# Kernel optimization log

Hardware: AMD Instinct MI355X
Metric: run time of the kernel (lower is better)

Reference implementation:

```python
import jax, jax.numpy as jnp
import numpy as np

# Module hyperparameters (from init_kwargs)
THRESHOLD_BASE = 1.0
TAU_MEM, TAU_SYN, TAU_ADAPT = 0.02, 0.005, 0.1
ADAPT_STRENGTH, HOMEO_RATE, DT = 0.1, 0.01, 0.001


def setup_inputs() -> dict:
    key = jax.random.key(0)
    B, F, T = 32, 8192, 128
    input_current = jax.random.normal(key, (B, F, T), dtype=jnp.float32)
    threshold_scale = jnp.ones((1,), dtype=jnp.float32)   # nn.Parameter(torch.ones(1))
    adaptation_bias = jnp.zeros((1,), dtype=jnp.float32)  # nn.Parameter(torch.zeros(1))
    return {"input_current": input_current,
            "threshold_scale": threshold_scale,
            "adaptation_bias": adaptation_bias}


def reference(input_current, threshold_scale, adaptation_bias):
    """Adaptive-threshold LIF neuron recurrence (AdaptiveThresholdLIFNeuron.forward).

    input_current: [B, F, T]
    Returns (spikes [B,F,T], membrane_trace [T], threshold_trace [T],
             final_firing_rate (scalar EMA), adaptation_state (scalar mean)).
    """
    B, F, T = input_current.shape
    dt = jnp.float32(DT)
    alpha = jnp.exp(-dt / TAU_MEM)   # membrane decay
    beta = jnp.exp(-dt / TAU_SYN)    # synaptic decay
    gamma = jnp.exp(-dt / TAU_ADAPT) # adaptation decay

    I_t = jnp.moveaxis(input_current, -1, 0)  # [T, B, F] for scan over time

    def step(carry, inp):
        membrane, synaptic, adaptation, ema = carry
        synaptic = beta * synaptic + inp
        membrane = alpha * membrane + synaptic
        # homeostatic component uses the running firing-rate EMA (scalar buffer)
        homeo = ADAPT_STRENGTH * jnp.maximum(ema - HOMEO_RATE, 0.0)
        adaptation = gamma * adaptation + (1.0 - gamma) * jax.lax.stop_gradient(membrane)
        threshold = (THRESHOLD_BASE * threshold_scale + homeo
                     + adaptation_bias + 0.1 * adaptation)  # [B, F]
        spike = (membrane >= threshold).astype(membrane.dtype)
        ema = 0.99 * ema + 0.01 * spike.mean()
        membrane = membrane - threshold * spike  # soft reset
        return (membrane, synaptic, adaptation, ema), (spike, membrane.mean(), threshold.mean())

    z = jnp.zeros((B, F), dtype=input_current.dtype)
    init = (z, z, z, jnp.zeros((), dtype=input_current.dtype))
    (membrane, synaptic, adaptation, ema), (spikes_t, mem_trace, thr_trace) = jax.lax.scan(step, init, I_t)

    spikes = jnp.moveaxis(spikes_t, 0, -1)  # [B, F, T]
    return spikes, mem_trace, thr_trace, ema, adaptation.mean()
```

## Files before the change

### kernel.cpp

```cpp
#include <hip/hip_runtime.h>
#include <math.h>

#pragma clang fp contract(off)

typedef unsigned int u32;

#define N_NEUR 262144
#define TT     128
#define OB     ((size_t)N_NEUR * TT)
#define PB     128
#define PT     512
#define NW     8
#define GUARD_MAX (1 << 16)

__device__ __forceinline__ float f4c(const float4 v, int c) {
  switch (c & 3) { case 0: return v.x; case 1: return v.y; case 2: return v.z; default: return v.w; }
}
__device__ __forceinline__ float wredf(float v) {
#pragma unroll
  for (int o = 32; o; o >>= 1) v += __shfl_xor(v, o);
  return v;
}
__device__ __forceinline__ int wredi(int v) {
#pragma unroll
  for (int o = 32; o; o >>= 1) v += __shfl_xor(v, o);
  return v;
}

__launch_bounds__(PT)
__global__ void snn_persist(const float* __restrict__ in, const float* __restrict__ tsp,
                            const float* __restrict__ abp, float* __restrict__ out,
                            u32* __restrict__ bits2, u32* __restrict__ g_cnt,
                            u32* __restrict__ g_tot, float* __restrict__ wm,
                            float* __restrict__ wt, float* __restrict__ wa)
{
#pragma clang fp contract(off)
  const int tid  = threadIdx.x;
  const int bid  = blockIdx.x;
  const int gtid = bid * PT + tid;
  const int lane = tid & 63;
  const int wv   = tid >> 6;

  const float alp = __uint_as_float(0x3F7383C5u);
  const float bet = __uint_as_float(0x3F519856u);
  const float gma = __uint_as_float(0x3F7D73E8u);
  const float omg = 1.0f - gma;
  const float tsv = tsp[0];
  const float abv = abp[0];

  float s0=0.f,s1=0.f,s2=0.f,s3=0.f;
  float m0=0.f,m1=0.f,m2=0.f,m3=0.f;
  float a0=0.f,a1=0.f,a2=0.f,a3=0.f;
  float ema = 0.f;
  float sc  = (tsv + 0.1f * fmaxf(ema - 0.01f, 0.0f)) + abv;

  __shared__ int   shc[NW];
  __shared__ float shm[NW];
  __shared__ u32   s_tot;

  const int n0 = gtid * 4;
  const float* r0 = in + (size_t)(n0 + 0) * TT;
  const float* r1 = in + (size_t)(n0 + 1) * TT;
  const float* r2 = in + (size_t)(n0 + 2) * TT;
  const float* r3 = in + (size_t)(n0 + 3) * TT;

#define STEPSYNC(I0, I1, I2, I3, T_) {                                         \
    s0 = __builtin_fmaf(bet, s0, (I0));                                        \
    m0 = __builtin_fmaf(alp, m0, s0);                                          \
    const float aw0 = omg * m0;                                                \
    a0 = __builtin_fmaf(gma, a0, aw0);                                         \
    const float th0 = __builtin_fmaf(0.1f, a0, sc);                            \
    const bool sp0 = (m0 >= th0); if (sp0) m0 = m0 - th0;                      \
    s1 = __builtin_fmaf(bet, s1, (I1));                                        \
    m1 = __builtin_fmaf(alp, m1, s1);                                          \
    const float aw1 = omg * m1;                                                \
    a1 = __builtin_fmaf(gma, a1, aw1);                                         \
    const float th1 = __builtin_fmaf(0.1f, a1, sc);                            \
    const bool sp1 = (m1 >= th1); if (sp1) m1 = m1 - th1;                      \
    s2 = __builtin_fmaf(bet, s2, (I2));                                        \
    m2 = __builtin_fmaf(alp, m2, s2);                                          \
    const float aw2 = omg * m2;                                                \
    a2 = __builtin_fmaf(gma, a2, aw2);                                         \
    const float th2 = __builtin_fmaf(0.1f, a2, sc);                            \
    const bool sp2 = (m2 >= th2); if (sp2) m2 = m2 - th2;                      \
    s3 = __builtin_fmaf(bet, s3, (I3));                                        \
    m3 = __builtin_fmaf(alp, m3, s3);                                          \
    const float aw3 = omg * m3;                                                \
    a3 = __builtin_fmaf(gma, a3, aw3);                                         \
    const float th3 = __builtin_fmaf(0.1f, a3, sc);                            \
    const bool sp3 = (m3 >= th3); if (sp3) m3 = m3 - th3;                      \
    int cnt = (int)sp0 + (int)sp1 + (int)sp2 + (int)sp3;                       \
    cnt = wredi(cnt);                                                          \
    if (lane == 0) shc[wv] = cnt;                                              \
    __syncthreads();                                                           \
    if (wv == 0 && lane == 0) {                                                \
      int bc = ((((((shc[0] + shc[1]) + shc[2]) + shc[3]) + shc[4])            \
                 + shc[5]) + shc[6]) + shc[7];                                 \
      __hip_atomic_store(&g_cnt[(size_t)(T_) * PB + bid], (u32)bc + 1u,        \
                         __ATOMIC_RELAXED, __HIP_MEMORY_SCOPE_AGENT);          \
    }                                                                          \
           \
    u32 nib = (u32)sp0 | ((u32)sp1 << 1) | ((u32)sp2 << 2) | ((u32)sp3 << 3);  \
    u32 word = nib << (4 * (tid & 7));                                         \
    word |= (u32)__shfl_xor((int)word, 1);                                     \
    word |= (u32)__shfl_xor((int)word, 2);                                     \
    word |= (u32)__shfl_xor((int)word, 4);                                     \
    if ((tid & 7) == 0) bits2[(size_t)(gtid >> 3) * TT + (T_)] = word;         \
    float msum = ((m0 + m1) + m2) + m3;                                        \
    float tsum = ((th0 + th1) + th2) + th3;                                    \
    msum = wredf(msum); tsum = wredf(tsum);                                    \
    if (lane == 0) {                                                           \
      wm[((size_t)(T_) * PB + bid) * NW + wv] = msum;                          \
      wt[((size_t)(T_) * PB + bid) * NW + wv] = tsum;                          \
    }                                                                          \
    if (wv == 0) {                                                             \
      if (bid == 0) {         \
        const u32* slots_ = g_cnt + (size_t)(T_) * PB;                         \
        u32 v0_, v1_; int gd_ = 0;                                             \
        while (1) {                                                            \
          v0_ = __hip_atomic_load(&slots_[lane],      __ATOMIC_RELAXED, __HIP_MEMORY_SCOPE_AGENT); \
          v1_ = __hip_atomic_load(&slots_[lane + 64], __ATOMIC_RELAXED, __HIP_MEMORY_SCOPE_AGENT); \
          if (__all(v0_ != 0u && v1_ != 0u)) break;                            \
          if (++gd_ > GUARD_MAX) break;                                        \
        }                                                                      \
        int ss_ = (int)(v0_ ? v0_ - 1u : 0u) + (int)(v1_ ? v1_ - 1u : 0u);     \
        ss_ = wredi(ss_);                                                      \
        if (lane == 0) {                                                       \
          __hip_atomic_store(&g_tot[(T_)], (u32)ss_ + 1u,                      \
                             __ATOMIC_RELAXED, __HIP_MEMORY_SCOPE_AGENT);      \
          s_tot = (u32)ss_;                                                    \
        }                                                                      \
      } else {           \
        u32 v_; int gd_ = 0;                                                   \
        while (1) {                                                            \
          v_ = __hip_atomic_load(&g_tot[(T_)], __ATOMIC_RELAXED, __HIP_MEMORY_SCOPE_AGENT); \
          if (v_ != 0u) break;                                                 \
          if (++gd_ > GUARD_MAX) break;                                        \
          __builtin_amdgcn_s_sleep(1);                                         \
        }                                                                      \
        if (lane == 0) s_tot = (v_ ? v_ - 1u : 0u);                            \
      }                                                                        \
    }                                                                          \
    __syncthreads();                                                           \
    const float mean_ = (float)s_tot * 3.814697265625e-06f;                    \
    ema = __builtin_fmaf(0.99f, ema, 0.01f * mean_);                           \
    sc  = (tsv + 0.1f * fmaxf(ema - 0.01f, 0.0f)) + abv;                       \
  }

#define LOADC(X0,X1,X2,X3,X4,X5,X6,X7, c) {            \
    X0 = *(const float4*)(r0 + (c) * 8);               \
    X1 = *(const float4*)(r0 + (c) * 8 + 4);           \
    X2 = *(const float4*)(r1 + (c) * 8);               \
    X3 = *(const float4*)(r1 + (c) * 8 + 4);           \
    X4 = *(const float4*)(r2 + (c) * 8);               \
    X5 = *(const float4*)(r2 + (c) * 8 + 4);           \
    X6 = *(const float4*)(r3 + (c) * 8);               \
    X7 = *(const float4*)(r3 + (c) * 8 + 4); }

#define DOCHUNK(X0,X1,X2,X3,X4,X5,X6,X7, c) {                     \
    _Pragma("unroll")                                             \
    for (int k = 0; k < 8; ++k) {                                 \
      const float i0_ = (k < 4) ? f4c(X0, k) : f4c(X1, k);        \
      const float i1_ = (k < 4) ? f4c(X2, k) : f4c(X3, k);        \
      const float i2_ = (k < 4) ? f4c(X4, k) : f4c(X5, k);        \
      const float i3_ = (k < 4) ? f4c(X6, k) : f4c(X7, k);        \
      STEPSYNC(i0_, i1_, i2_, i3_, (c) * 8 + k);                  \
    } }

  float4 A0,A1,A2,A3,A4,A5,A6,A7;
  float4 B0,B1,B2,B3,B4,B5,B6,B7;

  LOADC(A0,A1,A2,A3,A4,A5,A6,A7, 0);
  for (int cc = 0; cc < 8; ++cc) {
    LOADC(B0,B1,B2,B3,B4,B5,B6,B7, 2 * cc + 1);
    DOCHUNK(A0,A1,A2,A3,A4,A5,A6,A7, 2 * cc);
    if (cc < 7) LOADC(A0,A1,A2,A3,A4,A5,A6,A7, 2 * cc + 2);
    DOCHUNK(B0,B1,B2,B3,B4,B5,B6,B7, 2 * cc + 1);
  }
#undef DOCHUNK
#undef LOADC
#undef STEPSYNC

  float asum = ((a0 + a1) + a2) + a3;
  asum = wredf(asum);
  __syncthreads();
  if (lane == 0) shm[wv] = asum;
  __syncthreads();
  if (tid == 0) {
    float bs = 0.f;
    for (int w = 0; w < NW; ++w) bs += shm[w];
    wa[bid] = bs;
    if (bid == 0) out[OB + 256] = ema;
  }
}

__launch_bounds__(256)
__global__ void snn_finish(const float* __restrict__ wm, const float* __restrict__ wt,
                           const float* __restrict__ wa, float* __restrict__ out)
{
#pragma clang fp contract(off)
  const int tid = threadIdx.x;
  const float inv = 3.814697265625e-06f;
  if (tid < 128) {
    float s = 0.f;
    for (int j = 0; j < PB * NW; ++j) s += wm[(size_t)tid * PB * NW + j];
    out[OB + tid] = s * inv;
  } else {
    const int t = tid - 128;
    float s = 0.f;
    for (int j = 0; j < PB * NW; ++j) s += wt[(size_t)t * PB * NW + j];
    out[OB + 128 + t] = s * inv;
  }
  if (tid == 0) {
    float s = 0.f;
    for (int b = 0; b < PB; ++b) s += wa[b];
    out[OB + 257] = s * inv;
  }
}

__global__ void snn_expand(const u32* __restrict__ bits2, float* __restrict__ outF)
{
  const int gtid = blockIdx.x * blockDim.x + threadIdx.x;
  const int wave = gtid >> 6, lane = gtid & 63;
  const int nwaves = (gridDim.x * blockDim.x) >> 6;
  const int nloc = lane >> 5;
  const int tq   = lane & 31;
  for (int pair = wave; pair < N_NEUR / 2; pair += nwaves) {
    const int n = 2 * pair + nloc;
    const uint4 w = *(const uint4*)(bits2 + (size_t)(n >> 5) * TT + 4 * tq);
    const int b = n & 31;
    float4 f;
    f.x = (float)((w.x >> b) & 1u);
    f.y = (float)((w.y >> b) & 1u);
    f.z = (float)((w.z >> b) & 1u);
    f.w = (float)((w.w >> b) & 1u);
    ((float4*)outF)[(size_t)n * (TT / 4) + tq] = f;
  }
}

extern "C" void kernel_launch(void* const* d_in, const int* in_sizes, int n_in,
                              void* d_out, int out_size, void* d_ws, size_t ws_size,
                              hipStream_t stream)
{
  const float* in  = (const float*)d_in[0];
  const float* tsp = (const float*)d_in[1];
  const float* abp = (const float*)d_in[2];
  float* out = (float*)d_out;
  unsigned char* ws = (unsigned char*)d_ws;

  if (ws_size < 5310000u) return;

  u32*   bits2 = (u32*)(ws);
  float* wm    = (float*)(ws + 4194304);
  float* wt    = (float*)(ws + 4718592);
  u32*   g_cnt = (u32*)(ws + 5242880);
  u32*   g_tot = (u32*)(ws + 5308416);
  float* wa    = (float*)(ws + 5308928);

  hipMemsetAsync(g_cnt, 0, 66048, stream);

  snn_persist<<<dim3(PB), dim3(PT), 0, stream>>>(in, tsp, abp, out,
                                                 bits2, g_cnt, g_tot, wm, wt, wa);
  snn_finish<<<dim3(1), dim3(256), 0, stream>>>(wm, wt, wa, out);
  snn_expand<<<dim3(2048), dim3(256), 0, stream>>>(bits2, out);
}
```

Measured before the change: 392.1 us.

## Replace two-stage gather/broadcast grid barrier with single packed atomic counter

Each block now does one atomic add per timestep on a single per-step word. The add packs an arrival count in the low 8 bits and the block's spike count in the upper bits. All blocks then poll that one word until the arrival count reaches the block count. This removes the old scheme in which block 0 gathered per-block slots and republished the total, cutting one serialized cross-block hop from each of the 128 timesteps. In exchange, all blocks contend on one address for both the atomics and the polling.

```diff
diff --git a/kernel.cpp b/kernel.cpp
--- a/kernel.cpp
+++ b/kernel.cpp
@@ -30,9 +30,9 @@
 __launch_bounds__(PT)
 __global__ void snn_persist(const float* __restrict__ in, const float* __restrict__ tsp,
                             const float* __restrict__ abp, float* __restrict__ out,
-                            u32* __restrict__ bits2, u32* __restrict__ g_cnt,
-                            u32* __restrict__ g_tot, float* __restrict__ wm,
-                            float* __restrict__ wt, float* __restrict__ wa)
+                            u32* __restrict__ bits2, u32* __restrict__ g_acc,
+                            float* __restrict__ wm, float* __restrict__ wt,
+                            float* __restrict__ wa)
 {
 #pragma clang fp contract(off)
   const int tid  = threadIdx.x;
@@ -96,8 +96,8 @@
     if (wv == 0 && lane == 0) {                                                \
       int bc = ((((((shc[0] + shc[1]) + shc[2]) + shc[3]) + shc[4])            \
                  + shc[5]) + shc[6]) + shc[7];                                 \
-      __hip_atomic_store(&g_cnt[(size_t)(T_) * PB + bid], (u32)bc + 1u,        \
-                         __ATOMIC_RELAXED, __HIP_MEMORY_SCOPE_AGENT);          \
+      __hip_atomic_fetch_add(&g_acc[(T_)], 1u | ((u32)bc << 8),                \
+                             __ATOMIC_RELAXED, __HIP_MEMORY_SCOPE_AGENT);      \
     }                                                                          \
            \
     u32 nib = (u32)sp0 | ((u32)sp1 << 1) | ((u32)sp2 << 2) | ((u32)sp3 << 3);  \
@@ -113,33 +113,16 @@
       wm[((size_t)(T_) * PB + bid) * NW + wv] = msum;                          \
       wt[((size_t)(T_) * PB + bid) * NW + wv] = tsum;                          \
     }                                                                          \
-    if (wv == 0) {                                                             \
-      if (bid == 0) {         \
-        const u32* slots_ = g_cnt + (size_t)(T_) * PB;                         \
-        u32 v0_, v1_; int gd_ = 0;                                             \
-        while (1) {                                                            \
-          v0_ = __hip_atomic_load(&slots_[lane],      __ATOMIC_RELAXED, __HIP_MEMORY_SCOPE_AGENT); \
-          v1_ = __hip_atomic_load(&slots_[lane + 64], __ATOMIC_RELAXED, __HIP_MEMORY_SCOPE_AGENT); \
-          if (__all(v0_ != 0u && v1_ != 0u)) break;                            \
-          if (++gd_ > GUARD_MAX) break;                                        \
-        }                                                                      \
-        int ss_ = (int)(v0_ ? v0_ - 1u : 0u) + (int)(v1_ ? v1_ - 1u : 0u);     \
-        ss_ = wredi(ss_);                                                      \
-        if (lane == 0) {                                                       \
-          __hip_atomic_store(&g_tot[(T_)], (u32)ss_ + 1u,                      \
-                             __ATOMIC_RELAXED, __HIP_MEMORY_SCOPE_AGENT);      \
-          s_tot = (u32)ss_;                                                    \
-        }                                                                      \
-      } else {           \
-        u32 v_; int gd_ = 0;                                                   \
-        while (1) {                                                            \
-          v_ = __hip_atomic_load(&g_tot[(T_)], __ATOMIC_RELAXED, __HIP_MEMORY_SCOPE_AGENT); \
-          if (v_ != 0u) break;                                                 \
-          if (++gd_ > GUARD_MAX) break;                                        \
-          __builtin_amdgcn_s_sleep(1);                                         \
-        }                                                                      \
-        if (lane == 0) s_tot = (v_ ? v_ - 1u : 0u);                            \
+    if (wv == 0 && lane == 0) {                                                \
+      u32 v_; int gd_ = 0;                                                     \
+      while (1) {                                                              \
+        v_ = __hip_atomic_load(&g_acc[(T_)], __ATOMIC_RELAXED,                 \
+                               __HIP_MEMORY_SCOPE_AGENT);                      \
+        if ((v_ & 0xFFu) == (u32)PB) break;                                    \
+        if (++gd_ > GUARD_MAX) break;                                          \
+        __builtin_amdgcn_s_sleep(1);                                           \
       }                                                                        \
+      s_tot = v_ >> 8;                                                         \
     }                                                                          \
     __syncthreads();                                                           \
     const float mean_ = (float)s_tot * 3.814697265625e-06f;                    \
@@ -248,19 +231,18 @@
   float* out = (float*)d_out;
   unsigned char* ws = (unsigned char*)d_ws;
 
-  if (ws_size < 5310000u) return;
+  if (ws_size < 5244000u) return;
 
   u32*   bits2 = (u32*)(ws);
   float* wm    = (float*)(ws + 4194304);
   float* wt    = (float*)(ws + 4718592);
-  u32*   g_cnt = (u32*)(ws + 5242880);
-  u32*   g_tot = (u32*)(ws + 5308416);
-  float* wa    = (float*)(ws + 5308928);
-
-  hipMemsetAsync(g_cnt, 0, 66048, stream);
+  u32*   g_acc = (u32*)(ws + 5242880);
+  float* wa    = (float*)(ws + 5243392);
+
+  hipMemsetAsync(g_acc, 0, 512, stream);
 
   snn_persist<<<dim3(PB), dim3(PT), 0, stream>>>(in, tsp, abp, out,
-                                                 bits2, g_cnt, g_tot, wm, wt, wa);
+                                                 bits2, g_acc, wm, wt, wa);
   snn_finish<<<dim3(1), dim3(256), 0, stream>>>(wm, wt, wa, out);
   snn_expand<<<dim3(2048), dim3(256), 0, stream>>>(bits2, out);
 }
```

Result: slower. 460.3 us (+17.4%).
